# Kernel tuning notes

Hardware: AMD Instinct MI355X
Metric: run time of the kernel (lower is better)

## Reference

```python
import jax, jax.numpy as jnp
import numpy as np

N_NODES = 100000
N_EDGES = 3200000


def _gat_conv(x, src, dst, ea, Wx, We, a_src, a_dst, a_edge, b, n):
    # PyG GATConv, heads=1, edge_dim set: h = x@Wx^T, he = ea@We^T
    h = x @ Wx.T                      # [N,16]
    he = ea @ We.T                    # [E,16]
    alpha = h[src] @ a_src + h[dst] @ a_dst + he @ a_edge  # [E]
    alpha = jnp.where(alpha > 0, alpha, 0.2 * alpha)       # leaky_relu(0.2)
    m = jax.ops.segment_max(alpha, dst, num_segments=n)
    m = jnp.where(jnp.isfinite(m), m, 0.0)
    ex = jnp.exp(alpha - m[dst])
    s = jax.ops.segment_sum(ex, dst, num_segments=n)
    a = ex / (s[dst] + 1e-16)
    out = jax.ops.segment_sum(a[:, None] * h[src], dst, num_segments=n)
    return out + b


def setup_inputs() -> dict:
    key = jax.random.key(0)
    ks = iter(jax.random.split(key, 40))
    rn = lambda shape, s=0.1: jax.random.normal(next(ks), shape, dtype=jnp.float32) * s
    inp = {}
    inp['x'] = jax.random.normal(next(ks), (N_NODES, 4), dtype=jnp.float32)
    inp['edge_index'] = jax.random.randint(next(ks), (2, N_EDGES), 0, N_NODES, dtype=jnp.int64)
    inp['edge_attr'] = jax.random.normal(next(ks), (N_EDGES, 6), dtype=jnp.float32)
    # conv1: GATConv(4->16, edge_dim=6)
    inp['c1_Wx'] = rn((16, 4)); inp['c1_We'] = rn((16, 6))
    inp['c1_asrc'] = rn((16,)); inp['c1_adst'] = rn((16,)); inp['c1_aedge'] = rn((16,))
    inp['c1_b'] = rn((16,))
    # edge1 MLP: 38->32->64->32->16
    inp['e1_w1'] = rn((32, 38)); inp['e1_b1'] = rn((32,))
    inp['e1_w2'] = rn((64, 32)); inp['e1_b2'] = rn((64,))
    inp['e1_w3'] = rn((32, 64)); inp['e1_b3'] = rn((32,))
    inp['e1_w4'] = rn((16, 32)); inp['e1_b4'] = rn((16,))
    # conv2: GATConv(16->16, edge_dim=16)
    inp['c2_Wx'] = rn((16, 16)); inp['c2_We'] = rn((16, 16))
    inp['c2_asrc'] = rn((16,)); inp['c2_adst'] = rn((16,)); inp['c2_aedge'] = rn((16,))
    inp['c2_b'] = rn((16,))
    # node head 16->16->2, edge head 16->16->4
    inp['nl_w1'] = rn((16, 16)); inp['nl_b1'] = rn((16,))
    inp['nl_w2'] = rn((2, 16)); inp['nl_b2'] = rn((2,))
    inp['el_w1'] = rn((16, 16)); inp['el_b1'] = rn((16,))
    inp['el_w2'] = rn((4, 16)); inp['el_b2'] = rn((4,))
    return inp


def reference(x, edge_index, edge_attr,
              c1_Wx, c1_We, c1_asrc, c1_adst, c1_aedge, c1_b,
              e1_w1, e1_b1, e1_w2, e1_b2, e1_w3, e1_b3, e1_w4, e1_b4,
              c2_Wx, c2_We, c2_asrc, c2_adst, c2_aedge, c2_b,
              nl_w1, nl_b1, nl_w2, nl_b2,
              el_w1, el_b1, el_w2, el_b2):
    n = x.shape[0]
    src, dst = edge_index[0], edge_index[1]
    x1 = _gat_conv(x, src, dst, edge_attr, c1_Wx, c1_We, c1_asrc, c1_adst, c1_aedge, c1_b, n)
    # edge MLP on [x_src | edge_attr | x_dst] (dropout = identity in eval)
    e = jnp.concatenate([x1[src], edge_attr, x1[dst]], axis=1)  # [E,38]
    e = jax.nn.relu(e @ e1_w1.T + e1_b1)
    e = jax.nn.relu(e @ e1_w2.T + e1_b2)
    e = jax.nn.relu(e @ e1_w3.T + e1_b3)
    e = e @ e1_w4.T + e1_b4                                     # [E,16]
    x2 = _gat_conv(x1, src, dst, e, c2_Wx, c2_We, c2_asrc, c2_adst, c2_aedge, c2_b, n)
    node = jax.nn.relu(jax.nn.relu(x2 @ nl_w1.T + nl_b1) @ nl_w2.T + nl_b2)
    edge = jax.nn.relu(jax.nn.relu(e @ el_w1.T + el_b1) @ el_w2.T + el_b2)
    return (jax.nn.log_softmax(node, axis=1), jax.nn.log_softmax(edge, axis=1))
```

## Files before the change

kernel.cpp:

```cpp
#include <hip/hip_runtime.h>

#define NN 100000
#define NE 3200000
#define NB 98

typedef unsigned int u32;
typedef unsigned short u16;
typedef _Float16 f16x2 __attribute__((ext_vector_type(2)));
typedef _Float16 f16x8 __attribute__((ext_vector_type(8)));
typedef float fltx4 __attribute__((ext_vector_type(4)));
typedef __fp16 fp16v2 __attribute__((ext_vector_type(2)));

__device__ __forceinline__ int clampi(int s){
  s = s < 0 ? 0 : s;
  return s >= NN ? NN-1 : s;
}

__device__ __forceinline__ f16x2 pk2(float x, float y){
  fp16v2 r = __builtin_amdgcn_cvt_pkrtz(x, y);
  return __builtin_bit_cast(f16x2, r);
}
__device__ __forceinline__ u32 pk2u(float x, float y){
  return __builtin_bit_cast(u32, pk2(x, y));
}
__device__ __forceinline__ float dot2(f16x2 a, f16x2 b, float c){
  return __builtin_amdgcn_fdot2(a, b, c, false);
}
__device__ __forceinline__ float f16lo(u32 w){
  __fp16 h = __builtin_bit_cast(__fp16, (u16)(w & 0xffffu));
  return (float)h;
}
__device__ __forceinline__ float f16hi(u32 w){
  __fp16 h = __builtin_bit_cast(__fp16, (u16)(w >> 16));
  return (float)h;
}
__device__ __forceinline__ float f16u(u16 w){
  __fp16 h = __builtin_bit_cast(__fp16, w);
  return (float)h;
}

__global__ __launch_bounds__(256,8) void khist(const int* __restrict__ ei, int* __restrict__ cnt){
  int i = blockIdx.x*256 + threadIdx.x;
  if (i >= NE) return;
  atomicAdd(&cnt[clampi(ei[NE+i])], 1);
}

__global__ __launch_bounds__(1024) void kscanA(const int* __restrict__ cnt, int* __restrict__ bsum){
  __shared__ int wsum[16];
  int tid = threadIdx.x;
  int i = blockIdx.x*1024 + tid;
  int x = (i < NN) ? cnt[i] : 0;
  #pragma unroll
  for (int ofs = 1; ofs < 64; ofs <<= 1) x += __shfl_xor(x, ofs, 64);
  if ((tid & 63) == 0) wsum[tid >> 6] = x;
  __syncthreads();
  if (tid == 0){
    int t = 0;
    #pragma unroll
    for (int k = 0; k < 16; k++) t += wsum[k];
    bsum[blockIdx.x] = t;
  }
}

__global__ void kscanB(const int* __restrict__ bsum, int* __restrict__ boff, int* __restrict__ offN){
  if (threadIdx.x == 0){
    int c = 0;
    for (int b = 0; b < NB; b++){ boff[b] = c; c += bsum[b]; }
    offN[0] = c;
  }
}

__global__ __launch_bounds__(1024) void kscanC(int* __restrict__ cnt, const int* __restrict__ boff,
                                               int* __restrict__ off){
  __shared__ int wsum[16];
  int tid = threadIdx.x;
  int i = blockIdx.x*1024 + tid;
  int v = (i < NN) ? cnt[i] : 0;
  int x = v;
  #pragma unroll
  for (int ofs = 1; ofs < 64; ofs <<= 1){
    int t = __shfl_up(x, ofs, 64);
    if ((tid & 63) >= ofs) x += t;
  }
  if ((tid & 63) == 63) wsum[tid >> 6] = x;
  __syncthreads();
  if (tid < 16){
    int y = wsum[tid];
    #pragma unroll
    for (int ofs = 1; ofs < 16; ofs <<= 1){
      int t = __shfl_up(y, ofs, 64);
      if (tid >= ofs) y += t;
    }
    wsum[tid] = y;
  }
  __syncthreads();
  int wb = (tid >= 64) ? wsum[(tid >> 6) - 1] : 0;
  if (i < NN){ off[i] = boff[blockIdx.x] + wb + x - v; cnt[i] = 0; }
}

__global__ __launch_bounds__(256,4) void k1(const float* __restrict__ x,
    const float* __restrict__ Wx, const float* __restrict__ asrc, const float* __restrict__ adst,
    float* __restrict__ hs1, float* __restrict__ hd1)
{
  __shared__ float wL[64], aS[16], aD[16];
  int tid = threadIdx.x;
  if (tid < 64) wL[tid] = Wx[tid];
  if (tid < 16){ aS[tid] = asrc[tid]; aD[tid] = adst[tid]; }
  __syncthreads();
  int n = blockIdx.x*256 + tid;
  if (n >= NN) return;
  float4 xr = ((const float4*)x)[n];
  float hs=0.f, hd=0.f;
  #pragma unroll
  for (int j=0;j<16;j++){
    float h = xr.x*wL[j*4+0] + xr.y*wL[j*4+1] + xr.z*wL[j*4+2] + xr.w*wL[j*4+3];
    hs += h*aS[j]; hd += h*aD[j];
  }
  hs1[n]=hs; hd1[n]=hd;
}

__global__ __launch_bounds__(256,8) void k2a(const int* __restrict__ ei,
    const float* __restrict__ ea, const float* __restrict__ We, const float* __restrict__ aedge,
    const float* __restrict__ hs1, const float* __restrict__ hd1,
    const int* __restrict__ off, int* __restrict__ cnt, float2* __restrict__ edata)
{
  __shared__ float w6[6];
  int tid = threadIdx.x;
  if (tid < 6){
    float acc = 0.f;
    for (int j=0;j<16;j++) acc += aedge[j] * We[j*6+tid];
    w6[tid] = acc;
  }
  __syncthreads();
  int i = blockIdx.x*256 + tid;
  if (i >= NE) return;
  int s = clampi(ei[i]);
  int d = clampi(ei[NE + i]);
  const float2* eap = (const float2*)ea + (size_t)i*3;
  float2 u0 = eap[0], u1 = eap[1], u2 = eap[2];
  float al = hs1[s] + hd1[d]
    + u0.x*w6[0] + u0.y*w6[1] + u1.x*w6[2]
    + u1.y*w6[3] + u2.x*w6[4] + u2.y*w6[5];
  al = al > 0.f ? al : 0.2f*al;
  float ex = __expf(al);
  int pos = off[d] + atomicAdd(&cnt[d], 1);
  edata[pos] = make_float2(ex, __int_as_float(s));
}

__global__ __launch_bounds__(256,8) void k34(const float2* __restrict__ edata,
    const int* __restrict__ off, const float* __restrict__ x,
    const float* __restrict__ c1b, const float* __restrict__ Wx1, const float* __restrict__ Wx2,
    const float* __restrict__ a2s, const float* __restrict__ a2d,
    const float* __restrict__ w1p,
    u32* __restrict__ hpk, float* __restrict__ hs2, float* __restrict__ hd2,
    u32* __restrict__ uh, u32* __restrict__ vh, int* __restrict__ cnt)
{
  __shared__ float w0L[64], bL[16], wL[256], aS[16], aD[16];
  __shared__ float w1sL[32*16], w1dL[32*16];
  int tid = threadIdx.x;
  wL[tid] = Wx2[tid];
  if (tid < 64) w0L[tid] = Wx1[tid];
  if (tid < 16){ bL[tid]=c1b[tid]; aS[tid]=a2s[tid]; aD[tid]=a2d[tid]; }
  for (int idx=tid; idx<512; idx+=256){
    int j=idx>>4, k=idx&15;
    w1sL[idx] = w1p[j*38+k];
    w1dL[idx] = w1p[j*38+22+k];
  }
  __syncthreads();
  int t = blockIdx.x*256 + tid;
  int n = t >> 4;
  int j = t & 15;
  if (n >= NN) return;
  int f = j & 3, ks = j >> 2;
  int beg = off[n], end = off[n+1];
  float aj = 0.f, sl = 0.f;
  for (int k = beg + ks; k < end; k += 4){
    float2 p = edata[k];
    int src = __float_as_int(p.y);
    aj += p.x * x[(size_t)src*4 + f];
    sl += p.x;
  }
  aj += __shfl_xor(aj, 4, 64); aj += __shfl_xor(aj, 8, 64);
  sl += __shfl_xor(sl, 4, 64); sl += __shfl_xor(sl, 8, 64);
  float inv = 1.f/(sl + 1e-16f);
  float m0 = __shfl(aj, 0, 16)*inv;
  float m1 = __shfl(aj, 1, 16)*inv;
  float m2 = __shfl(aj, 2, 16)*inv;
  float m3 = __shfl(aj, 3, 16)*inv;
  float xvj = m0*w0L[j*4+0] + m1*w0L[j*4+1] + m2*w0L[j*4+2] + m3*w0L[j*4+3] + bL[j];
  float hv = 0.f, u0=0.f, u1=0.f, v0=0.f, v1=0.f;
  #pragma unroll
  for (int k=0;k<16;k++){
    float vk = __shfl(xvj, k, 16);
    hv += vk * wL[j*16+k];
    u0 += vk * w1sL[(2*j)*16+k];
    u1 += vk * w1sL[(2*j+1)*16+k];
    v0 += vk * w1dL[(2*j)*16+k];
    v1 += vk * w1dL[(2*j+1)*16+k];
  }
  ((u16*)hpk)[(size_t)n*16 + j] = (u16)(pk2u(hv, 0.f) & 0xffffu);
  uh[(size_t)n*16 + j] = pk2u(u0, u1);
  vh[(size_t)n*16 + j] = pk2u(v0, v1);
  float hsp = hv*aS[j], hdp = hv*aD[j];
  #pragma unroll
  for (int ofs=1; ofs<16; ofs<<=1){
    hsp += __shfl_xor(hsp, ofs, 64);
    hdp += __shfl_xor(hdp, ofs, 64);
  }
  if (j == 0){ hs2[n]=hsp; hd2[n]=hdp; cnt[n]=0; }
}

__global__ __launch_bounds__(256,4) void k5m(
    const int* __restrict__ ei, const float* __restrict__ ea,
    const u32* __restrict__ uh, const u32* __restrict__ vh,
    const float* __restrict__ hs2, const float* __restrict__ hd2,
    const float* w1p, const float* b1p, const float* w2p, const float* b2p,
    const float* w3p, const float* b3p, const float* w4p, const float* b4p,
    const float* We2, const float* a2e,
    const float* ew1p, const float* eb1p, const float* ew2p, const float* eb2p,
    const int* __restrict__ off, int* __restrict__ cnt, float2* __restrict__ edata,
    float* __restrict__ eout)
{
  __shared__ __align__(16) u32 a13L[4][1024];
  __shared__ __align__(16) u32 a2L[4][512];
  __shared__ __align__(16) uint4 b2f[4][64];
  __shared__ __align__(16) uint4 b3f[4][64];
  __shared__ __align__(16) f16x2 w1eh[32*4];  __shared__ float b1L[32];
  __shared__ float b2L[64], b3L[32];
  __shared__ __align__(16) f16x2 M1h[16*16];  __shared__ float c1L[16];
  __shared__ __align__(16) f16x2 ew2h[4*8];   __shared__ float eb2L[4];
  __shared__ __align__(16) f16x2 w16w4h[16];
  __shared__ float w16L[16];  __shared__ float w16b4L;

  int tid = threadIdx.x;
  if (tid < 128){
    int j=tid>>2, kk=tid&3;
    int k0=2*kk, k1=2*kk+1;
    float v0 = (k0<6) ? w1p[j*38+16+k0] : 0.f;
    float v1 = (k1<6) ? w1p[j*38+16+k1] : 0.f;
    w1eh[tid] = pk2(v0, v1);
  }
  {
    int c = tid>>6, l = tid&63;
    int j = c*16 + (l&15), kb = (l>>4)*8;
    const float* src = w2p + j*32 + kb;
    uint4 q;
    q.x = pk2u(src[0], src[1]); q.y = pk2u(src[2], src[3]);
    q.z = pk2u(src[4], src[5]); q.w = pk2u(src[6], src[7]);
    b2f[c][l] = q;
  }
  {
    int kt = tid>>7, c = (tid>>6)&1, l = tid&63;
    int j = c*16 + (l&15), kb = kt*32 + (l>>4)*8;
    const float* src = w3p + j*64 + kb;
    uint4 q;
    q.x = pk2u(src[0], src[1]); q.y = pk2u(src[2], src[3]);
    q.z = pk2u(src[4], src[5]); q.w = pk2u(src[6], src[7]);
    b3f[kt*2+c][l] = q;
  }
  if (tid < 64) b2L[tid] = b2p[tid];
  if (tid < 32){ b1L[tid] = b1p[tid]; b3L[tid] = b3p[tid]; }
  {
    int o = tid>>4, p = tid&15;
    float m0=0.f, m1=0.f;
    #pragma unroll
    for (int q=0;q<16;q++){
      float w = ew1p[o*16+q];
      m0 += w * w4p[q*32 + 2*p];
      m1 += w * w4p[q*32 + 2*p + 1];
    }
    M1h[o*16+p] = pk2(m0, m1);
  }
  if (tid < 16){
    float acc = eb1p[tid];
    for (int q=0;q<16;q++) acc += ew1p[tid*16+q]*b4p[q];
    c1L[tid] = acc;
    float w=0.f;
    for (int j=0;j<16;j++) w += a2e[j] * We2[j*16+tid];
    w16L[tid] = w;
  }
  if (tid < 32){
    int j=tid>>3, kk=tid&7;
    ew2h[tid] = pk2(ew2p[j*16+2*kk], ew2p[j*16+2*kk+1]);
  }
  if (tid < 4) eb2L[tid] = eb2p[tid];
  __syncthreads();
  if (tid < 16){
    float s0=0.f, s1=0.f;
    for (int q=0;q<16;q++){
      s0 += w16L[q]*w4p[q*32 + 2*tid];
      s1 += w16L[q]*w4p[q*32 + 2*tid + 1];
    }
    w16w4h[tid] = pk2(s0, s1);
  }
  if (tid == 0){
    float acc=0.f;
    for (int q=0;q<16;q++) acc += w16L[q]*b4p[q];
    w16b4L = acc;
  }
  __syncthreads();

  int wid = tid>>6, lane = tid&63;
  int cl = lane & 15, g = lane >> 4;
  u32* a13 = a13L[wid];
  u32* a2u = a2L[wid];
  int i = blockIdx.x*256 + tid;
  int s = clampi(ei[i]);
  int d = clampi(ei[NE + i]);

  u32 a1h[16];
  {
    const float2* eap = (const float2*)ea + (size_t)i*3;
    float2 e0=eap[0], e1=eap[1], e2=eap[2];
    f16x2 eh[4];
    eh[0]=pk2(e0.x,e0.y); eh[1]=pk2(e1.x,e1.y); eh[2]=pk2(e2.x,e2.y); eh[3]=pk2(0.f,0.f);
    const uint4* up = (const uint4*)(uh + (size_t)s*16);
    const uint4* vp = (const uint4*)(vh + (size_t)d*16);
    uint4 U[4], V[4];
    #pragma unroll
    for (int q=0;q<4;q++){ U[q]=up[q]; V[q]=vp[q]; }
    u32 uw[16], vw[16];
    #pragma unroll
    for (int q=0;q<4;q++){
      uw[4*q]=U[q].x; uw[4*q+1]=U[q].y; uw[4*q+2]=U[q].z; uw[4*q+3]=U[q].w;
      vw[4*q]=V[q].x; vw[4*q+1]=V[q].y; vw[4*q+2]=V[q].z; vw[4*q+3]=V[q].w;
    }
    #pragma unroll
    for (int j=0;j<16;j++){
      float t0 = b1L[2*j]   + f16lo(uw[j]) + f16lo(vw[j]);
      float t1 = b1L[2*j+1] + f16hi(uw[j]) + f16hi(vw[j]);
      #pragma unroll
      for (int kk=0;kk<4;kk++){
        t0 = dot2(eh[kk], w1eh[(2*j)*4+kk],   t0);
        t1 = dot2(eh[kk], w1eh[(2*j+1)*4+kk], t1);
      }
      a1h[j] = pk2u(fmaxf(t0,0.f), fmaxf(t1,0.f));
    }
  }
  {
    uint4* dst = (uint4*)(a13 + lane*16);
    dst[0] = make_uint4(a1h[0],a1h[1],a1h[2],a1h[3]);
    dst[1] = make_uint4(a1h[4],a1h[5],a1h[6],a1h[7]);
    dst[2] = make_uint4(a1h[8],a1h[9],a1h[10],a1h[11]);
    dst[3] = make_uint4(a1h[12],a1h[13],a1h[14],a1h[15]);
  }
  f16x8 fb2[4], fb3[4];
  #pragma unroll
  for (int c=0;c<4;c++) fb2[c] = __builtin_bit_cast(f16x8, b2f[c][lane]);
  #pragma unroll
  for (int q=0;q<4;q++) fb3[q] = __builtin_bit_cast(f16x8, b3f[q][lane]);
  __syncthreads();

  #pragma unroll
  for (int r=0;r<4;r++){
    __syncthreads();
    uint4 av = *(const uint4*)(a13 + (r*16 + cl)*16 + g*4);
    f16x8 af = __builtin_bit_cast(f16x8, av);
    _Float16* a2h_ = (_Float16*)a2u;
    #pragma unroll
    for (int c=0;c<4;c++){
      float b = b2L[c*16 + cl];
      fltx4 acc = {b,b,b,b};
      acc = __builtin_amdgcn_mfma_f32_16x16x32_f16(af, fb2[c], acc, 0, 0, 0);
      int col = c*16 + cl;
      int rowb = g*4;
      a2h_[(rowb+0)*64 + col] = (_Float16)fmaxf(acc[0], 0.f);
      a2h_[(rowb+1)*64 + col] = (_Float16)fmaxf(acc[1], 0.f);
      a2h_[(rowb+2)*64 + col] = (_Float16)fmaxf(acc[2], 0.f);
      a2h_[(rowb+3)*64 + col] = (_Float16)fmaxf(acc[3], 0.f);
    }
    __syncthreads();
    uint4 a20 = *(const uint4*)(a2u + cl*32 + g*4);
    uint4 a21 = *(const uint4*)(a2u + cl*32 + 16 + g*4);
    f16x8 af0 = __builtin_bit_cast(f16x8, a20);
    f16x8 af1 = __builtin_bit_cast(f16x8, a21);
    _Float16* a3w = (_Float16*)a13;
    #pragma unroll
    for (int c=0;c<2;c++){
      float b = b3L[c*16 + cl];
      fltx4 acc = {b,b,b,b};
      acc = __builtin_amdgcn_mfma_f32_16x16x32_f16(af0, fb3[0*2+c], acc, 0, 0, 0);
      acc = __builtin_amdgcn_mfma_f32_16x16x32_f16(af1, fb3[1*2+c], acc, 0, 0, 0);
      int col = c*16 + cl;
      int row = r*16 + g*4;
      a3w[(row+0)*32 + col] = (_Float16)fmaxf(acc[0], 0.f);
      a3w[(row+1)*32 + col] = (_Float16)fmaxf(acc[1], 0.f);
      a3w[(row+2)*32 + col] = (_Float16)fmaxf(acc[2], 0.f);
      a3w[(row+3)*32 + col] = (_Float16)fmaxf(acc[3], 0.f);
    }
  }
  __syncthreads();
  u32 a3h[16];
  {
    const uint4* srcp = (const uint4*)(a13 + lane*16);
    uint4 q0=srcp[0], q1=srcp[1], q2=srcp[2], q3=srcp[3];
    a3h[0]=q0.x; a3h[1]=q0.y; a3h[2]=q0.z; a3h[3]=q0.w;
    a3h[4]=q1.x; a3h[5]=q1.y; a3h[6]=q1.z; a3h[7]=q1.w;
    a3h[8]=q2.x; a3h[9]=q2.y; a3h[10]=q2.z; a3h[11]=q2.w;
    a3h[12]=q3.x; a3h[13]=q3.y; a3h[14]=q3.z; a3h[15]=q3.w;
  }
  f16x2 th[8];
  #pragma unroll
  for (int o=0;o<8;o++){
    float t0 = c1L[2*o], t1 = c1L[2*o+1];
    #pragma unroll
    for (int kp=0;kp<16;kp++){
      f16x2 a = __builtin_bit_cast(f16x2, a3h[kp]);
      t0 = dot2(a, M1h[(2*o)*16+kp],   t0);
      t1 = dot2(a, M1h[(2*o+1)*16+kp], t1);
    }
    th[o] = pk2(fmaxf(t0,0.f), fmaxf(t1,0.f));
  }
  float y0 = eb2L[0], y1 = eb2L[1], y2 = eb2L[2], y3 = eb2L[3];
  #pragma unroll
  for (int kk=0;kk<8;kk++){
    y0 = dot2(th[kk], ew2h[0*8+kk], y0);
    y1 = dot2(th[kk], ew2h[1*8+kk], y1);
    y2 = dot2(th[kk], ew2h[2*8+kk], y2);
    y3 = dot2(th[kk], ew2h[3*8+kk], y3);
  }
  y0 = fmaxf(y0,0.f); y1 = fmaxf(y1,0.f); y2 = fmaxf(y2,0.f); y3 = fmaxf(y3,0.f);
  float m = fmaxf(fmaxf(y0,y1), fmaxf(y2,y3));
  float l = m + __logf(__expf(y0-m)+__expf(y1-m)+__expf(y2-m)+__expf(y3-m));
  float4 eo; eo.x = y0-l; eo.y = y1-l; eo.z = y2-l; eo.w = y3-l;
  ((float4*)eout)[i] = eo;

  float al = hs2[s] + hd2[d] + w16b4L;
  #pragma unroll
  for (int kp=0;kp<16;kp++){
    f16x2 a = __builtin_bit_cast(f16x2, a3h[kp]);
    al = dot2(a, w16w4h[kp], al);
  }
  al = al > 0.f ? al : 0.2f*al;
  float ex = __expf(al);
  int pos = off[d] + atomicAdd(&cnt[d], 1);
  edata[pos] = make_float2(ex, __int_as_float(s));
}

__global__ __launch_bounds__(256,8) void kagg2(const float2* __restrict__ edata,
    const int* __restrict__ off, const u16* __restrict__ hpk,
    const float* __restrict__ c2b,
    const float* __restrict__ w1p, const float* __restrict__ b1p,
    const float* __restrict__ w2p, const float* __restrict__ b2p,
    float* __restrict__ nout, int* __restrict__ cnt)
{
  __shared__ float w1L[256], cb[16], b1L[16], w2L[32], b2L[2];
  int tid = threadIdx.x;
  w1L[tid] = w1p[tid];
  if (tid < 16){ cb[tid] = c2b[tid]; b1L[tid] = b1p[tid]; }
  if (tid < 32) w2L[tid] = w2p[tid];
  if (tid < 2)  b2L[tid] = b2p[tid];
  __syncthreads();
  int t = blockIdx.x*256 + tid;
  int n = t >> 6;
  int l = t & 63;
  if (n >= NN) return;
  int j = l & 15, ks = l >> 4;
  int beg = off[n], end = off[n+1];
  float aj = 0.f, sl = 0.f;
  for (int k = beg + ks; k < end; k += 4){
    float2 p = edata[k];
    int src = __float_as_int(p.y);
    aj += p.x * f16u(hpk[(size_t)src*16 + j]);
    sl += p.x;
  }
  aj += __shfl_xor(aj, 16, 64); aj += __shfl_xor(aj, 32, 64);
  sl += __shfl_xor(sl, 16, 64); sl += __shfl_xor(sl, 32, 64);
  float inv = 1.f/(sl + 1e-16f);
  float vj = aj*inv + cb[j];
  float tj = b1L[j];
  #pragma unroll
  for (int k=0;k<16;k++){
    float vk = __shfl(vj, k, 16);
    tj += vk * w1L[j*16 + k];
  }
  tj = fmaxf(tj, 0.f);
  float p0 = tj * w2L[j];
  float p1 = tj * w2L[16 + j];
  #pragma unroll
  for (int ofs=1; ofs<16; ofs<<=1){
    p0 += __shfl_xor(p0, ofs, 64);
    p1 += __shfl_xor(p1, ofs, 64);
  }
  if (l == 0){
    float y0 = fmaxf(p0 + b2L[0], 0.f);
    float y1 = fmaxf(p1 + b2L[1], 0.f);
    float m = fmaxf(y0, y1);
    float lg = m + __logf(__expf(y0-m) + __expf(y1-m));
    float2 no; no.x = y0-lg; no.y = y1-lg;
    ((float2*)nout)[n] = no;
    cnt[n] = 0;
  }
}

extern "C" void kernel_launch(void* const* d_in, const int* in_sizes, int n_in,
                              void* d_out, int out_size, void* d_ws, size_t ws_size,
                              hipStream_t stream)
{
  const float* x  = (const float*)d_in[0];
  const int* ei   = (const int*)d_in[1];
  const float* ea = (const float*)d_in[2];
  const float* c1Wx = (const float*)d_in[3];
  const float* c1We = (const float*)d_in[4];
  const float* c1as = (const float*)d_in[5];
  const float* c1ad = (const float*)d_in[6];
  const float* c1ae = (const float*)d_in[7];
  const float* c1b  = (const float*)d_in[8];
  const float* e1w1 = (const float*)d_in[9];
  const float* e1b1 = (const float*)d_in[10];
  const float* e1w2 = (const float*)d_in[11];
  const float* e1b2 = (const float*)d_in[12];
  const float* e1w3 = (const float*)d_in[13];
  const float* e1b3 = (const float*)d_in[14];
  const float* e1w4 = (const float*)d_in[15];
  const float* e1b4 = (const float*)d_in[16];
  const float* c2Wx = (const float*)d_in[17];
  const float* c2We = (const float*)d_in[18];
  const float* c2as = (const float*)d_in[19];
  const float* c2ad = (const float*)d_in[20];
  const float* c2ae = (const float*)d_in[21];
  const float* c2b  = (const float*)d_in[22];
  const float* nlw1 = (const float*)d_in[23];
  const float* nlb1 = (const float*)d_in[24];
  const float* nlw2 = (const float*)d_in[25];
  const float* nlb2 = (const float*)d_in[26];
  const float* elw1 = (const float*)d_in[27];
  const float* elb1 = (const float*)d_in[28];
  const float* elw2 = (const float*)d_in[29];
  const float* elb2 = (const float*)d_in[30];

  float* ws = (float*)d_ws;
  const size_t N = NN;
  int* off   = (int*)ws;
  int* cnt   = (int*)ws + (N + 8);
  int* bsum  = (int*)ws + (2*N + 8);
  int* boff  = (int*)ws + (2*N + 136);
  u32* hpk   = (u32*)(ws + 2*N + 264);
  float* hs  = ws + 10*N + 264;
  float* hd  = hs + N;
  u32* uh    = (u32*)(hd + N);
  u32* vh    = uh + 16*N;
  float2* edata = (float2*)(vh + 16*N);

  float* nout = (float*)d_out;
  float* eout = (float*)d_out + 200000;

  const int GE = (NE + 255)/256;
  const int GN = (NN + 255)/256;

  (void)hipMemsetAsync(cnt, 0, N*sizeof(int), stream);
  khist<<<GE, 256, 0, stream>>>(ei, cnt);
  kscanA<<<NB, 1024, 0, stream>>>(cnt, bsum);
  kscanB<<<1, 64, 0, stream>>>(bsum, boff, off + NN);
  kscanC<<<NB, 1024, 0, stream>>>(cnt, boff, off);
  k1<<<GN, 256, 0, stream>>>(x, c1Wx, c1as, c1ad, hs, hd);
  k2a<<<GE, 256, 0, stream>>>(ei, ea, c1We, c1ae, hs, hd, off, cnt, edata);
  k34<<<(NN*16 + 255)/256, 256, 0, stream>>>(edata, off, x,
      c1b, c1Wx, c2Wx, c2as, c2ad, e1w1, hpk, hs, hd, uh, vh, cnt);
  k5m<<<GE, 256, 0, stream>>>(ei, ea, uh, vh, hs, hd,
      e1w1, e1b1, e1w2, e1b2, e1w3, e1b3, e1w4, e1b4,
      c2We, c2ae, elw1, elb1, elw2, elb2,
      off, cnt, edata, eout);
  kagg2<<<(NN*64 + 255)/256, 256, 0, stream>>>(edata, off, (const u16*)hpk,
      c2b, nlw1, nlb1, nlw2, nlb2, nout, cnt);
}
```

Measured before the change: 742.3 us.

## Replace block barriers with wave-local waits and pad LDS tiles in edge MLP

In the fused edge-MLP kernel, the block-wide __syncthreads calls around each wave's private LDS staging buffers become wave-level lgkmcnt waits with a scheduling barrier. The activation tiles get padded row strides to reduce LDS bank conflicts. The MFMA B-fragments for layers 2 and 3 are now built per lane directly from global weights instead of going through shared memory. The intent is to remove block barrier stalls and conflicts, at the cost of redundant global weight loads per wave and reliance on wave-lockstep LDS visibility for correctness.

```diff
diff --git a/kernel.cpp b/kernel.cpp
--- a/kernel.cpp
+++ b/kernel.cpp
@@ -37,6 +37,10 @@
 __device__ __forceinline__ float f16u(u16 w){
   __fp16 h = __builtin_bit_cast(__fp16, w);
   return (float)h;
+}
+__device__ __forceinline__ void wsync(){
+  asm volatile("s_waitcnt lgkmcnt(0)" ::: "memory");
+  __builtin_amdgcn_sched_barrier(0);
 }
 
 __global__ __launch_bounds__(256,8) void khist(const int* __restrict__ ei, int* __restrict__ cnt){
@@ -210,6 +214,8 @@
   if (j == 0){ hs2[n]=hsp; hd2[n]=hdp; cnt[n]=0; }
 }
 
+#define A13S 20
+#define A2S  36
 __global__ __launch_bounds__(256,4) void k5m(
     const int* __restrict__ ei, const float* __restrict__ ea,
     const u32* __restrict__ uh, const u32* __restrict__ vh,
@@ -221,10 +227,8 @@
     const int* __restrict__ off, int* __restrict__ cnt, float2* __restrict__ edata,
     float* __restrict__ eout)
 {
-  __shared__ __align__(16) u32 a13L[4][1024];
-  __shared__ __align__(16) u32 a2L[4][512];
-  __shared__ __align__(16) uint4 b2f[4][64];
-  __shared__ __align__(16) uint4 b3f[4][64];
+  __shared__ __align__(16) u32 a13L[4][64*A13S];
+  __shared__ __align__(16) u32 a2L[4][16*A2S];
   __shared__ __align__(16) f16x2 w1eh[32*4];  __shared__ float b1L[32];
   __shared__ float b2L[64], b3L[32];
   __shared__ __align__(16) f16x2 M1h[16*16];  __shared__ float c1L[16];
@@ -239,24 +243,6 @@
     float v0 = (k0<6) ? w1p[j*38+16+k0] : 0.f;
     float v1 = (k1<6) ? w1p[j*38+16+k1] : 0.f;
     w1eh[tid] = pk2(v0, v1);
-  }
-  {
-    int c = tid>>6, l = tid&63;
-    int j = c*16 + (l&15), kb = (l>>4)*8;
-    const float* src = w2p + j*32 + kb;
-    uint4 q;
-    q.x = pk2u(src[0], src[1]); q.y = pk2u(src[2], src[3]);
-    q.z = pk2u(src[4], src[5]); q.w = pk2u(src[6], src[7]);
-    b2f[c][l] = q;
-  }
-  {
-    int kt = tid>>7, c = (tid>>6)&1, l = tid&63;
-    int j = c*16 + (l&15), kb = kt*32 + (l>>4)*8;
-    const float* src = w3p + j*64 + kb;
-    uint4 q;
-    q.x = pk2u(src[0], src[1]); q.y = pk2u(src[2], src[3]);
-    q.z = pk2u(src[4], src[5]); q.w = pk2u(src[6], src[7]);
-    b3f[kt*2+c][l] = q;
   }
   if (tid < 64) b2L[tid] = b2p[tid];
   if (tid < 32){ b1L[tid] = b1p[tid]; b3L[tid] = b3p[tid]; }
@@ -307,6 +293,26 @@
   int i = blockIdx.x*256 + tid;
   int s = clampi(ei[i]);
   int d = clampi(ei[NE + i]);
+
+  f16x8 fb2[4], fb3[4];
+  #pragma unroll
+  for (int c=0;c<4;c++){
+    const float* src = w2p + (c*16 + cl)*32 + g*8;
+    uint4 q;
+    q.x = pk2u(src[0], src[1]); q.y = pk2u(src[2], src[3]);
+    q.z = pk2u(src[4], src[5]); q.w = pk2u(src[6], src[7]);
+    fb2[c] = __builtin_bit_cast(f16x8, q);
+  }
+  #pragma unroll
+  for (int kt=0;kt<2;kt++)
+  #pragma unroll
+  for (int c=0;c<2;c++){
+    const float* src = w3p + (c*16 + cl)*64 + kt*32 + g*8;
+    uint4 q;
+    q.x = pk2u(src[0], src[1]); q.y = pk2u(src[2], src[3]);
+    q.z = pk2u(src[4], src[5]); q.w = pk2u(src[6], src[7]);
+    fb3[kt*2+c] = __builtin_bit_cast(f16x8, q);
+  }
 
   u32 a1h[16];
   {
@@ -338,23 +344,18 @@
     }
   }
   {
-    uint4* dst = (uint4*)(a13 + lane*16);
+    uint4* dst = (uint4*)(a13 + lane*A13S);
     dst[0] = make_uint4(a1h[0],a1h[1],a1h[2],a1h[3]);
     dst[1] = make_uint4(a1h[4],a1h[5],a1h[6],a1h[7]);
     dst[2] = make_uint4(a1h[8],a1h[9],a1h[10],a1h[11]);
     dst[3] = make_uint4(a1h[12],a1h[13],a1h[14],a1h[15]);
   }
-  f16x8 fb2[4], fb3[4];
-  #pragma unroll
-  for (int c=0;c<4;c++) fb2[c] = __builtin_bit_cast(f16x8, b2f[c][lane]);
-  #pragma unroll
-  for (int q=0;q<4;q++) fb3[q] = __builtin_bit_cast(f16x8, b3f[q][lane]);
-  __syncthreads();
+  wsync();
 
   #pragma unroll
   for (int r=0;r<4;r++){
-    __syncthreads();
-    uint4 av = *(const uint4*)(a13 + (r*16 + cl)*16 + g*4);
+    wsync();
+    uint4 av = *(const uint4*)(a13 + (r*16 + cl)*A13S + g*4);
     f16x8 af = __builtin_bit_cast(f16x8, av);
     _Float16* a2h_ = (_Float16*)a2u;
     #pragma unroll
@@ -364,14 +365,14 @@
       acc = __builtin_amdgcn_mfma_f32_16x16x32_f16(af, fb2[c], acc, 0, 0, 0);
       int col = c*16 + cl;
       int rowb = g*4;
-      a2h_[(rowb+0)*64 + col] = (_Float16)fmaxf(acc[0], 0.f);
-      a2h_[(rowb+1)*64 + col] = (_Float16)fmaxf(acc[1], 0.f);
-      a2h_[(rowb+2)*64 + col] = (_Float16)fmaxf(acc[2], 0.f);
-      a2h_[(rowb+3)*64 + col] = (_Float16)fmaxf(acc[3], 0.f);
-    }
-    __syncthreads();
-    uint4 a20 = *(const uint4*)(a2u + cl*32 + g*4);
-    uint4 a21 = *(const uint4*)(a2u + cl*32 + 16 + g*4);
+      a2h_[(rowb+0)*(2*A2S) + col] = (_Float16)fmaxf(acc[0], 0.f);
+      a2h_[(rowb+1)*(2*A2S) + col] = (_Float16)fmaxf(acc[1], 0.f);
+      a2h_[(rowb+2)*(2*A2S) + col] = (_Float16)fmaxf(acc[2], 0.f);
+      a2h_[(rowb+3)*(2*A2S) + col] = (_Float16)fmaxf(acc[3], 0.f);
+    }
+    wsync();
+    uint4 a20 = *(const uint4*)(a2u + cl*A2S + g*4);
+    uint4 a21 = *(const uint4*)(a2u + cl*A2S + 16 + g*4);
     f16x8 af0 = __builtin_bit_cast(f16x8, a20);
     f16x8 af1 = __builtin_bit_cast(f16x8, a21);
     _Float16* a3w = (_Float16*)a13;
@@ -383,16 +384,16 @@
       acc = __builtin_amdgcn_mfma_f32_16x16x32_f16(af1, fb3[1*2+c], acc, 0, 0, 0);
       int col = c*16 + cl;
       int row = r*16 + g*4;
-      a3w[(row+0)*32 + col] = (_Float16)fmaxf(acc[0], 0.f);
-      a3w[(row+1)*32 + col] = (_Float16)fmaxf(acc[1], 0.f);
-      a3w[(row+2)*32 + col] = (_Float16)fmaxf(acc[2], 0.f);
-      a3w[(row+3)*32 + col] = (_Float16)fmaxf(acc[3], 0.f);
-    }
-  }
-  __syncthreads();
+      a3w[(row+0)*(2*A13S) + col] = (_Float16)fmaxf(acc[0], 0.f);
+      a3w[(row+1)*(2*A13S) + col] = (_Float16)fmaxf(acc[1], 0.f);
+      a3w[(row+2)*(2*A13S) + col] = (_Float16)fmaxf(acc[2], 0.f);
+      a3w[(row+3)*(2*A13S) + col] = (_Float16)fmaxf(acc[3], 0.f);
+    }
+  }
+  wsync();
   u32 a3h[16];
   {
-    const uint4* srcp = (const uint4*)(a13 + lane*16);
+    const uint4* srcp = (const uint4*)(a13 + lane*A13S);
     uint4 q0=srcp[0], q1=srcp[1], q2=srcp[2], q3=srcp[3];
     a3h[0]=q0.x; a3h[1]=q0.y; a3h[2]=q0.z; a3h[3]=q0.w;
     a3h[4]=q1.x; a3h[5]=q1.y; a3h[6]=q1.z; a3h[7]=q1.w;
```

Result: slower. 776.5 us (+4.6%).
